# Kernel optimization log

Hardware: AMD Instinct MI355X
Metric: run time of the kernel (lower is better)

## Reference

```python
import jax, jax.numpy as jnp
import numpy as np

EMB = 1024
HEADS = 16
BLOCK = 128


def setup_inputs() -> dict:
    key = jax.random.key(0)
    k1, k2, k3 = jax.random.split(key, 3)
    B, T, C = 4, 4096, EMB
    x = jax.random.normal(k1, (B, T, C), dtype=jnp.float32)
    # Linear weights stored as [in, out] (i.e. torch W.T); qkv has no bias.
    W_qkv = jax.random.normal(k2, (C, 3 * C), dtype=jnp.float32) * 0.02
    W_proj = jax.random.normal(k3, (C, C), dtype=jnp.float32) * 0.02
    b_proj = jnp.zeros((C,), dtype=jnp.float32)
    return {"x": x, "W_qkv": W_qkv, "W_proj": W_proj, "b_proj": b_proj}


def reference(x, W_qkv, W_proj, b_proj):
    # Dropout is inference-mode identity.
    B, T, C = x.shape
    H, D, BS = HEADS, C // HEADS, BLOCK
    nb = T // BS  # number of local blocks
    qkv = x @ W_qkv  # [B,T,3C]
    q, k, v = jnp.split(qkv, 3, axis=-1)
    # [B, nb, BS, H, D] -- each block attends only within itself
    q = q.reshape(B, nb, BS, H, D)
    k = k.reshape(B, nb, BS, H, D)
    v = v.reshape(B, nb, BS, H, D)
    scores = jnp.einsum("bnqhd,bnkhd->bnhqk", q, k) / jnp.sqrt(jnp.float32(D))
    # is_decoder: causal tril within each diagonal block (tril[i:end, i:end])
    tril = jnp.tril(jnp.ones((BS, BS), dtype=bool))
    scores = jnp.where(tril, scores, -jnp.inf)
    # faithful to original: stable exp, then divide by (sum + 1e-6)
    scores = scores - jnp.max(scores, axis=-1, keepdims=True)
    e = jnp.exp(scores)
    p = e / (jnp.sum(e, axis=-1, keepdims=True) + 1e-6)
    out = jnp.einsum("bnhqk,bnkhd->bnqhd", p, v).reshape(B, T, C)
    return out @ W_proj + b_proj
```

## Files before the change

kernel.cpp:

```cpp
#include <hip/hip_runtime.h>
#include <hip/hip_bf16.h>
#include <math.h>


typedef __bf16 bf16_t;
typedef __bf16 bf16x8 __attribute__((ext_vector_type(8)));
typedef unsigned short u16x8 __attribute__((ext_vector_type(8)));
typedef float  f32x4  __attribute__((ext_vector_type(4)));

typedef const __attribute__((address_space(1))) void* gptr_t;
typedef __attribute__((address_space(3))) void* lptr_t;

__global__ __launch_bounds__(256) void prepass(const float* __restrict__ x,
                                               bf16_t* __restrict__ xb,
                                               const float* __restrict__ Wqkv,
                                               bf16_t* __restrict__ wqkvT,
                                               const float* __restrict__ Wproj,
                                               bf16_t* __restrict__ wprojT) {
    __shared__ float tile[32][33];
    const int bid = blockIdx.x;
    if (bid < 8192) {
        const size_t n = (size_t)16384 * 1024;
        const size_t stride = (size_t)8192 * 256 * 4;
        for (size_t i = ((size_t)bid * 256 + threadIdx.x) * 4; i < n; i += stride) {
            float4 v = *(const float4*)(x + i);
            bf16_t t[4];
            t[0] = (bf16_t)v.x; t[1] = (bf16_t)v.y; t[2] = (bf16_t)v.z; t[3] = (bf16_t)v.w;
            *(uint2*)(xb + i) = *(uint2*)t;
        }
        return;
    }
    const float* in;
    bf16_t* out;
    int K, N, bx, by;
    if (bid < 8192 + 3072) {
        const int t = bid - 8192;
        in = Wqkv; out = wqkvT; K = 1024; N = 3072;
        bx = t % 96; by = t / 96;
    } else {
        const int t = bid - 11264;
        in = Wproj; out = wprojT; K = 1024; N = 1024;
        bx = t & 31; by = t >> 5;
    }
    const int tx = threadIdx.x & 31, ty = threadIdx.x >> 5;
    #pragma unroll
    for (int i = 0; i < 4; i++) {
        const int k = by * 32 + ty + i * 8;
        tile[ty + i * 8][tx] = in[(size_t)k * N + bx * 32 + tx];
    }
    __syncthreads();
    #pragma unroll
    for (int i = 0; i < 4; i++) {
        const int n = bx * 32 + ty + i * 8;
        out[(size_t)n * K + by * 32 + tx] = (bf16_t)tile[tx][ty + i * 8];
    }
}

template <bool BF16_OUT, bool BIAS>
__global__ __launch_bounds__(1024, 4) void gemm256q(const bf16_t* __restrict__ A,
                                                    const bf16_t* __restrict__ Bt,
                                                    void* __restrict__ Cout,
                                                    const float* __restrict__ bias,
                                                    int M, int N, int K) {
    __shared__ bf16_t ring[3][16384];

    const int tid  = threadIdx.x;
    const int lane = tid & 63, wave = tid >> 6;
    const int quad = lane >> 4, l16 = lane & 15;
    const int wm = wave >> 2, wn = wave & 3;

    const int nbm  = M >> 8;
    const int mloc = nbm >> 3;
    const int xcd  = blockIdx.x & 7;
    const int idx  = blockIdx.x >> 3;
    const int bn   = idx / mloc;
    const int bm   = xcd * mloc + (idx - bn * mloc);

    const bf16_t* Ab = A  + (size_t)bm * 256 * K;
    const bf16_t* Bb = Bt + (size_t)bn * 256 * K;

    const int srow = lane >> 2;
    const int scs  = (lane & 3) ^ ((srow >> 1) & 3);
    const int rdo  = ((quad ^ ((l16 >> 1) & 3)) << 3);

    f32x4 acc[4][4];
    #pragma unroll
    for (int i = 0; i < 4; ++i)
        #pragma unroll
        for (int j = 0; j < 4; ++j) acc[i][j] = (f32x4){0.f, 0.f, 0.f, 0.f};

#define STG(SLICE, SLOT)                                                              \
    do {                                                                              \
        __builtin_amdgcn_global_load_lds(                                             \
            (gptr_t)(Ab + (size_t)(wave * 16 + srow) * K + ((SLICE) << 5) + scs * 8), \
            (lptr_t)&ring[SLOT][wave * 512], 16, 0, 0);                               \
        __builtin_amdgcn_global_load_lds(                                             \
            (gptr_t)(Bb + (size_t)(wave * 16 + srow) * K + ((SLICE) << 5) + scs * 8), \
            (lptr_t)&ring[SLOT][8192 + wave * 512], 16, 0, 0);                        \
    } while (0)

#define BODY(G, RS, SS, DO_STAGE, WAIT_STMT)                                          \
    do {                                                                              \
        const bf16_t* sl_ = ring[RS];                                                 \
        bf16x8 af_[4], bf_[4];                                                        \
        _Pragma("unroll")                                                             \
        for (int fr = 0; fr < 4; ++fr)                                                \
            af_[fr] = *(const bf16x8*)&sl_[(wm * 64 + fr * 16 + l16) * 32 + rdo];     \
        _Pragma("unroll")                                                             \
        for (int fr = 0; fr < 4; ++fr)                                                \
            bf_[fr] =                                                                 \
                *(const bf16x8*)&sl_[8192 + (wn * 64 + fr * 16 + l16) * 32 + rdo];    \
        if (DO_STAGE) STG((G) + 2, SS);                                               \
        WAIT_STMT;                                                                    \
        __builtin_amdgcn_s_barrier();                                                 \
        __builtin_amdgcn_s_setprio(1);                                                \
        _Pragma("unroll")                                                             \
        for (int mr = 0; mr < 4; ++mr)                                                \
            _Pragma("unroll")                                                         \
            for (int nr = 0; nr < 4; ++nr)                                            \
                acc[mr][nr] = __builtin_amdgcn_mfma_f32_16x16x32_bf16(                \
                    af_[mr], bf_[nr], acc[mr][nr], 0, 0, 0);                          \
        __builtin_amdgcn_s_setprio(0);                                                \
    } while (0)

    STG(0, 0); STG(1, 1);
    asm volatile("s_waitcnt vmcnt(2)" ::: "memory");
    __builtin_amdgcn_s_barrier();

    const int NS = K >> 5;
    int rs = 0, ss = 2;
    for (int g = 0; g < NS - 2; ++g) {
        BODY(g, rs, ss, true, asm volatile("s_waitcnt vmcnt(2)" ::: "memory"));
        rs = (rs == 2) ? 0 : rs + 1;
        ss = (ss == 2) ? 0 : ss + 1;
    }
    BODY(NS - 2, rs, ss, false, asm volatile("s_waitcnt vmcnt(0)" ::: "memory"));
    rs = (rs == 2) ? 0 : rs + 1;
    BODY(NS - 1, rs, ss, false, (void)0);
#undef BODY
#undef STG

    #pragma unroll
    for (int mr = 0; mr < 4; ++mr) {
        #pragma unroll
        for (int nr = 0; nr < 4; ++nr) {
            const int gcol = bn * 256 + wn * 64 + nr * 16 + l16;
            #pragma unroll
            for (int reg = 0; reg < 4; ++reg) {
                const int grow = bm * 256 + wm * 64 + mr * 16 + quad * 4 + reg;
                float v = acc[mr][nr][reg];
                if (BIAS) v += bias[gcol];
                if (BF16_OUT)
                    ((bf16_t*)Cout)[(size_t)grow * N + gcol] = (bf16_t)v;
                else
                    ((float*)Cout)[(size_t)grow * N + gcol] = v;
            }
        }
    }
}

__global__ __launch_bounds__(256, 3) void attn_kernel(const bf16_t* __restrict__ qkv,
                                                      bf16_t* __restrict__ attn_out) {
    __shared__ __align__(16) char smem[54272];
    bf16_t* qs = (bf16_t*)smem;
    bf16_t* ks = (bf16_t*)(smem + 18432);
    bf16_t* vT = (bf16_t*)(smem + 36864);
    bf16_t* ps = (bf16_t*)smem;

    const int tid = threadIdx.x;
    const int lane = tid & 63, wave = tid >> 6;
    const int quad = lane >> 4, l16 = lane & 15;

    const int gid = blockIdx.x;
    const int xcd = gid & 7;
    const int j = gid >> 3;
    const int h = j & 15;
    const int blkhi = (j >> 4) & 3;
    const int b = j >> 6;
    const int blk = blkhi * 8 + xcd;
    const int row0 = (b * 32 + blk) * 128;
    const int LDQ = 3072;

    for (int t = tid; t < 128 * 8; t += 256) {
        const int r = t >> 3;
        const int c = (t & 7) * 8;
        const bf16_t* src = qkv + (size_t)(row0 + r) * LDQ + h * 64;
        *(uint4*)&qs[r * 72 + c] = *(const uint4*)(src + c);
        *(uint4*)&ks[r * 72 + c] = *(const uint4*)(src + 1024 + c);
    }
    for (int t = tid; t < 64 * 8; t += 256) {
        const int r2 = t >> 3;
        const int c0 = (t & 7) * 8;
        const bf16_t* vsrc = qkv + (size_t)(row0 + 2 * r2) * LDQ + h * 64 + 2048 + c0;
        u16x8 v0 = *(const u16x8*)(vsrc);
        u16x8 v1 = *(const u16x8*)(vsrc + LDQ);
        const int X = (t & 7) << 3;
        #pragma unroll
        for (int jj = 0; jj < 8; jj++) {
            unsigned int pv = (unsigned int)v0[jj] | ((unsigned int)v1[jj] << 16);
            *(unsigned int*)&vT[(c0 + jj) * 136 + ((2 * r2) ^ X)] = pv;
        }
    }
    __syncthreads();

    f32x4 sfrag[2][8];
    for (int mr = 0; mr < 2; mr++)
        for (int nc = 0; nc < 8; nc++)
            sfrag[mr][nc] = (f32x4){0.f, 0.f, 0.f, 0.f};

    #pragma unroll
    for (int ksl = 0; ksl < 2; ksl++) {
        bf16x8 aq[2], bk[8];
        #pragma unroll
        for (int mr = 0; mr < 2; mr++)
            aq[mr] = *(const bf16x8*)&qs[(wave * 32 + mr * 16 + l16) * 72 + ksl * 32 + quad * 8];
        #pragma unroll
        for (int nc = 0; nc < 8; nc++)
            bk[nc] = *(const bf16x8*)&ks[(nc * 16 + l16) * 72 + ksl * 32 + quad * 8];
        #pragma unroll
        for (int mr = 0; mr < 2; mr++)
            #pragma unroll
            for (int nc = 0; nc < 8; nc++)
                sfrag[mr][nc] = __builtin_amdgcn_mfma_f32_16x16x32_bf16(aq[mr], bk[nc], sfrag[mr][nc], 0, 0, 0);
    }

    #pragma unroll
    for (int mr = 0; mr < 2; mr++) {
        #pragma unroll
        for (int nc = 0; nc < 8; nc++) {
            #pragma unroll
            for (int reg = 0; reg < 4; reg++) {
                const int row = wave * 32 + mr * 16 + quad * 4 + reg;
                const int col = nc * 16 + l16;
                float s = sfrag[mr][nc][reg] * 0.125f;
                if (col > row) s = -INFINITY;
                sfrag[mr][nc][reg] = s;
            }
        }
    }

    #pragma unroll
    for (int mr = 0; mr < 2; mr++) {
        #pragma unroll
        for (int reg = 0; reg < 4; reg++) {
            float m = -INFINITY;
            #pragma unroll
            for (int nc = 0; nc < 8; nc++) m = fmaxf(m, sfrag[mr][nc][reg]);
            #pragma unroll
            for (int off = 1; off < 16; off <<= 1) m = fmaxf(m, __shfl_xor(m, off));
            float sum = 0.f;
            #pragma unroll
            for (int nc = 0; nc < 8; nc++) {
                float e = __expf(sfrag[mr][nc][reg] - m);
                sfrag[mr][nc][reg] = e;
                sum += e;
            }
            #pragma unroll
            for (int off = 1; off < 16; off <<= 1) sum += __shfl_xor(sum, off);
            const float inv = 1.0f / (sum + 1e-6f);
            #pragma unroll
            for (int nc = 0; nc < 8; nc++) sfrag[mr][nc][reg] *= inv;
        }
    }

    __syncthreads();

    #pragma unroll
    for (int mr = 0; mr < 2; mr++)
        #pragma unroll
        for (int nc = 0; nc < 8; nc++)
            #pragma unroll
            for (int reg = 0; reg < 4; reg++) {
                const int row = wave * 32 + mr * 16 + quad * 4 + reg;
                const int col = nc * 16 + l16;
                ps[row * 136 + col] = (bf16_t)sfrag[mr][nc][reg];
            }
    __syncthreads();

    f32x4 oacc[2][4];
    for (int mr = 0; mr < 2; mr++)
        for (int nd = 0; nd < 4; nd++)
            oacc[mr][nd] = (f32x4){0.f, 0.f, 0.f, 0.f};

    #pragma unroll
    for (int ksl = 0; ksl < 4; ksl++) {
        bf16x8 ap[2];
        #pragma unroll
        for (int mr = 0; mr < 2; mr++)
            ap[mr] = *(const bf16x8*)&ps[(wave * 32 + mr * 16 + l16) * 136 + ksl * 32 + quad * 8];
        #pragma unroll
        for (int nd = 0; nd < 4; nd++) {
            const int c2 = nd * 16 + l16;
            const int X2 = ((c2 >> 3) & 7) << 3;
            bf16x8 bv = *(const bf16x8*)&vT[c2 * 136 + ((ksl * 32 + quad * 8) ^ X2)];
            #pragma unroll
            for (int mr = 0; mr < 2; mr++)
                oacc[mr][nd] = __builtin_amdgcn_mfma_f32_16x16x32_bf16(ap[mr], bv, oacc[mr][nd], 0, 0, 0);
        }
    }

    #pragma unroll
    for (int mr = 0; mr < 2; mr++)
        #pragma unroll
        for (int nd = 0; nd < 4; nd++)
            #pragma unroll
            for (int reg = 0; reg < 4; reg++) {
                const int row = row0 + wave * 32 + mr * 16 + quad * 4 + reg;
                const int col = h * 64 + nd * 16 + l16;
                attn_out[(size_t)row * 1024 + col] = (bf16_t)oacc[mr][nd][reg];
            }
}

extern "C" void kernel_launch(void* const* d_in, const int* in_sizes, int n_in,
                              void* d_out, int out_size, void* d_ws, size_t ws_size,
                              hipStream_t stream) {
    const float* x     = (const float*)d_in[0];
    const float* Wqkv  = (const float*)d_in[1];
    const float* Wproj = (const float*)d_in[2];
    const float* bproj = (const float*)d_in[3];

    const int M = 16384, C = 1024, N1 = 3072;

    char* ws = (char*)d_ws;
    bf16_t* xb     = (bf16_t*)(ws);
    bf16_t* wqkvT  = (bf16_t*)(ws + 33554432);
    bf16_t* wprojT = (bf16_t*)(ws + 39845888);
    bf16_t* qkvb   = (bf16_t*)(ws + 41943040);
    bf16_t* attnb  = (bf16_t*)(ws + 142606336);

    prepass<<<12288, 256, 0, stream>>>(x, xb, Wqkv, wqkvT, Wproj, wprojT);

    gemm256q<true, false><<<(N1 / 256) * (M / 256), 1024, 0, stream>>>(
        xb, wqkvT, (void*)qkvb, nullptr, M, N1, C);

    attn_kernel<<<2048, 256, 0, stream>>>(qkvb, attnb);

    gemm256q<false, true><<<(C / 256) * (M / 256), 1024, 0, stream>>>(
        attnb, wprojT, d_out, bproj, M, C, C);
}
```

Measured before the change: 300.9 us.

## Shrink attention LDS footprint: Q in registers, direct-to-LDS K, half P staging

The attention kernel now loads Q fragments straight from global memory into registers instead of staging them in shared memory. K is copied with global_load_lds into an XOR-swizzled unpadded layout. P is written to shared memory in two halves of 64 columns, each reused per wave without a block barrier. Shared memory drops from about 54KB to 35KB and launch bounds rise to 4 blocks per CU, aiming at higher occupancy and fewer barriers. The trade-off is higher register pressure and reliance on per-wave ordering of the P region written into the K buffer.

```diff
diff --git a/kernel.cpp b/kernel.cpp
--- a/kernel.cpp
+++ b/kernel.cpp
@@ -159,13 +159,12 @@
     }
 }
 
-__global__ __launch_bounds__(256, 3) void attn_kernel(const bf16_t* __restrict__ qkv,
+__global__ __launch_bounds__(256, 4) void attn_kernel(const bf16_t* __restrict__ qkv,
                                                       bf16_t* __restrict__ attn_out) {
-    __shared__ __align__(16) char smem[54272];
-    bf16_t* qs = (bf16_t*)smem;
-    bf16_t* ks = (bf16_t*)(smem + 18432);
-    bf16_t* vT = (bf16_t*)(smem + 36864);
+    __shared__ __align__(16) char smem[35840];
+    bf16_t* ks = (bf16_t*)smem;
     bf16_t* ps = (bf16_t*)smem;
+    bf16_t* vT = (bf16_t*)(smem + 18432);
 
     const int tid = threadIdx.x;
     const int lane = tid & 63, wave = tid >> 6;
@@ -181,12 +180,25 @@
     const int row0 = (b * 32 + blk) * 128;
     const int LDQ = 3072;
 
-    for (int t = tid; t < 128 * 8; t += 256) {
-        const int r = t >> 3;
-        const int c = (t & 7) * 8;
-        const bf16_t* src = qkv + (size_t)(row0 + r) * LDQ + h * 64;
-        *(uint4*)&qs[r * 72 + c] = *(const uint4*)(src + c);
-        *(uint4*)&ks[r * 72 + c] = *(const uint4*)(src + 1024 + c);
+    bf16x8 aq[2][2];
+    #pragma unroll
+    for (int mr = 0; mr < 2; mr++)
+        #pragma unroll
+        for (int ksl = 0; ksl < 2; ksl++)
+            aq[mr][ksl] = *(const bf16x8*)(qkv +
+                (size_t)(row0 + wave * 32 + mr * 16 + l16) * LDQ + h * 64 +
+                ksl * 32 + quad * 8);
+
+    {
+        const int r8 = lane >> 3;
+        const int cs = (lane & 7) ^ r8;
+        #pragma unroll
+        for (int i = 0; i < 4; i++) {
+            __builtin_amdgcn_global_load_lds(
+                (gptr_t)(qkv + (size_t)(row0 + i * 32 + wave * 8 + r8) * LDQ +
+                         1024 + h * 64 + cs * 8),
+                (lptr_t)&ks[(i * 32 + wave * 8) * 64], 16, 0, 0);
+        }
     }
     for (int t = tid; t < 64 * 8; t += 256) {
         const int r2 = t >> 3;
@@ -204,24 +216,25 @@
     __syncthreads();
 
     f32x4 sfrag[2][8];
+    #pragma unroll
     for (int mr = 0; mr < 2; mr++)
+        #pragma unroll
         for (int nc = 0; nc < 8; nc++)
             sfrag[mr][nc] = (f32x4){0.f, 0.f, 0.f, 0.f};
 
     #pragma unroll
     for (int ksl = 0; ksl < 2; ksl++) {
-        bf16x8 aq[2], bk[8];
+        bf16x8 bk[8];
+        #pragma unroll
+        for (int nc = 0; nc < 8; nc++)
+            bk[nc] = *(const bf16x8*)&ks[(nc * 16 + l16) * 64 +
+                                         (((ksl * 4 + quad) ^ (l16 & 7)) << 3)];
         #pragma unroll
         for (int mr = 0; mr < 2; mr++)
-            aq[mr] = *(const bf16x8*)&qs[(wave * 32 + mr * 16 + l16) * 72 + ksl * 32 + quad * 8];
-        #pragma unroll
-        for (int nc = 0; nc < 8; nc++)
-            bk[nc] = *(const bf16x8*)&ks[(nc * 16 + l16) * 72 + ksl * 32 + quad * 8];
-        #pragma unroll
-        for (int mr = 0; mr < 2; mr++)
             #pragma unroll
             for (int nc = 0; nc < 8; nc++)
-                sfrag[mr][nc] = __builtin_amdgcn_mfma_f32_16x16x32_bf16(aq[mr], bk[nc], sfrag[mr][nc], 0, 0, 0);
+                sfrag[mr][nc] = __builtin_amdgcn_mfma_f32_16x16x32_bf16(
+                    aq[mr][ksl], bk[nc], sfrag[mr][nc], 0, 0, 0);
     }
 
     #pragma unroll
@@ -265,37 +278,44 @@
 
     __syncthreads();
 
+    f32x4 oacc[2][4];
     #pragma unroll
     for (int mr = 0; mr < 2; mr++)
         #pragma unroll
-        for (int nc = 0; nc < 8; nc++)
-            #pragma unroll
-            for (int reg = 0; reg < 4; reg++) {
-                const int row = wave * 32 + mr * 16 + quad * 4 + reg;
-                const int col = nc * 16 + l16;
-                ps[row * 136 + col] = (bf16_t)sfrag[mr][nc][reg];
-            }
-    __syncthreads();
-
-    f32x4 oacc[2][4];
-    for (int mr = 0; mr < 2; mr++)
         for (int nd = 0; nd < 4; nd++)
             oacc[mr][nd] = (f32x4){0.f, 0.f, 0.f, 0.f};
 
     #pragma unroll
-    for (int ksl = 0; ksl < 4; ksl++) {
-        bf16x8 ap[2];
+    for (int half = 0; half < 2; half++) {
         #pragma unroll
         for (int mr = 0; mr < 2; mr++)
-            ap[mr] = *(const bf16x8*)&ps[(wave * 32 + mr * 16 + l16) * 136 + ksl * 32 + quad * 8];
-        #pragma unroll
-        for (int nd = 0; nd < 4; nd++) {
-            const int c2 = nd * 16 + l16;
-            const int X2 = ((c2 >> 3) & 7) << 3;
-            bf16x8 bv = *(const bf16x8*)&vT[c2 * 136 + ((ksl * 32 + quad * 8) ^ X2)];
+            #pragma unroll
+            for (int nc = 0; nc < 4; nc++)
+                #pragma unroll
+                for (int reg = 0; reg < 4; reg++) {
+                    const int row = wave * 32 + mr * 16 + quad * 4 + reg;
+                    ps[row * 72 + nc * 16 + l16] = (bf16_t)sfrag[mr][half * 4 + nc][reg];
+                }
+        asm volatile("s_waitcnt lgkmcnt(0)" ::: "memory");
+        __builtin_amdgcn_sched_barrier(0);
+        #pragma unroll
+        for (int kh = 0; kh < 2; kh++) {
+            const int G = half * 2 + kh;
+            bf16x8 ap[2];
             #pragma unroll
             for (int mr = 0; mr < 2; mr++)
-                oacc[mr][nd] = __builtin_amdgcn_mfma_f32_16x16x32_bf16(ap[mr], bv, oacc[mr][nd], 0, 0, 0);
+                ap[mr] = *(const bf16x8*)&ps[(wave * 32 + mr * 16 + l16) * 72 +
+                                             kh * 32 + quad * 8];
+            #pragma unroll
+            for (int nd = 0; nd < 4; nd++) {
+                const int c2 = nd * 16 + l16;
+                const int X2 = ((c2 >> 3) & 7) << 3;
+                bf16x8 bv = *(const bf16x8*)&vT[c2 * 136 + ((G * 32 + quad * 8) ^ X2)];
+                #pragma unroll
+                for (int mr = 0; mr < 2; mr++)
+                    oacc[mr][nd] = __builtin_amdgcn_mfma_f32_16x16x32_bf16(
+                        ap[mr], bv, oacc[mr][nd], 0, 0, 0);
+            }
         }
     }
 
```

Result: no change. 305.1 us (+1.4%).
